# Kernel tuning notes

Measured on AMD Instinct MI355X. Metric: run time of the kernel, lower is better.

The kernel has to match this reference:

```python
import jax, jax.numpy as jnp
import numpy as np

EPS = 1e-5


def _gcn_conv(x, src, dst, n_nodes, W, b):
    # x: [N, Fin]; src/dst: [E+N] (self-loops already appended)
    h = x @ W                                   # [N, Fout]
    deg = jnp.zeros((n_nodes,), x.dtype).at[dst].add(1.0)
    dinv = jax.lax.rsqrt(deg)                   # deg >= 1 due to self-loops
    norm = dinv[src] * dinv[dst]                # [E+N]
    msg = h[src] * norm[:, None]                # [E+N, Fout]  (gather)
    out = jax.ops.segment_sum(msg, dst, num_segments=n_nodes)  # scatter-add
    return out + b


def _bn_relu(x, gamma, beta):
    # BatchNorm over nodes (training-style batch statistics), then ReLU.
    mu = jnp.mean(x, axis=0)
    var = jnp.mean((x - mu) ** 2, axis=0)       # biased variance (torch BN)
    xn = (x - mu) * jax.lax.rsqrt(var + EPS)
    return jax.nn.relu(xn * gamma + beta)


def setup_inputs() -> dict:
    key = jax.random.key(0)
    ks = jax.random.split(key, 12)
    N, E, Fin, H, O, G = 100000, 1600000, 128, 128, 64, 128
    x = jax.random.normal(ks[0], (N, Fin), dtype=jnp.float32)
    edge_index = jax.random.randint(ks[1], (2, E), 0, N, dtype=jnp.int64)
    batch = jnp.sort(jax.random.randint(ks[2], (N,), 0, G, dtype=jnp.int64))
    s = 1.0 / np.sqrt(Fin)
    W0 = jax.random.uniform(ks[3], (Fin, H), jnp.float32, -s, s)
    b0 = jnp.zeros((H,), jnp.float32)
    g0 = jnp.ones((H,), jnp.float32)
    be0 = jnp.zeros((H,), jnp.float32)
    s2 = 1.0 / np.sqrt(H)
    W1 = jax.random.uniform(ks[4], (H, H), jnp.float32, -s2, s2)
    b1 = jnp.zeros((H,), jnp.float32)
    g1 = jnp.ones((H,), jnp.float32)
    be1 = jnp.zeros((H,), jnp.float32)
    Wout = jax.random.uniform(ks[5], (H, O), jnp.float32, -s2, s2)
    bout = jax.random.uniform(ks[6], (O,), jnp.float32, -s2, s2)
    return {"x": x, "edge_index": edge_index, "batch": batch, "num_graphs": 128,
            "W0": W0, "b0": b0, "g0": g0, "be0": be0,
            "W1": W1, "b1": b1, "g1": g1, "be1": be1,
            "Wout": Wout, "bout": bout}


def reference(x, edge_index, batch, num_graphs,
              W0, b0, g0, be0, W1, b1, g1, be1, Wout, bout):
    N = x.shape[0]
    loops = jnp.arange(N, dtype=edge_index.dtype)
    src = jnp.concatenate([edge_index[0], loops])  # add self-loops
    dst = jnp.concatenate([edge_index[1], loops])
    h = _gcn_conv(x, src, dst, N, W0, b0)
    h = _bn_relu(h, g0, be0)                       # Dropout(p=0.1) = identity in eval
    h = _gcn_conv(h, src, dst, N, W1, b1)
    h = _bn_relu(h, g1, be1)
    # global mean pool over graphs
    sums = jax.ops.segment_sum(h, batch, num_segments=num_graphs)   # [G, H]
    cnt = jax.ops.segment_sum(jnp.ones((N,), h.dtype), batch, num_segments=num_graphs)
    pooled = sums / jnp.maximum(cnt, 1.0)[:, None]
    return pooled @ Wout + bout
```

## Files before the change

### kernel.cpp

```cpp
#include <hip/hip_runtime.h>
#include <hip/hip_bf16.h>

typedef _Float16 half8_t __attribute__((ext_vector_type(8)));
typedef _Float16 half2_t __attribute__((ext_vector_type(2)));
typedef float float4_t __attribute__((ext_vector_type(4)));
typedef float float2_t __attribute__((ext_vector_type(2)));

#define WROW 136


__global__ __launch_bounds__(256) void k_hist(const int* __restrict__ dst, int E, int SH,
                                              int NBK, int WG, int CH, int* __restrict__ M) {
    extern __shared__ int lh[];
    for (int i = threadIdx.x; i < NBK; i += 256) lh[i] = 0;
    __syncthreads();
    int wg = blockIdx.x;
    int e0 = wg * CH, e1 = min(E, e0 + CH);
    for (int e = e0 + threadIdx.x; e < e1; e += 256)
        atomicAdd(&lh[dst[e] >> SH], 1);
    __syncthreads();
    for (int i = threadIdx.x; i < NBK; i += 256) M[i * WG + wg] = lh[i];
}

__global__ __launch_bounds__(256) void k_colscan(int* __restrict__ M, int WG,
                                                 int* __restrict__ totals) {
    __shared__ int s[256];
    int b = blockIdx.x, t = threadIdx.x;
    int v = (t < WG) ? M[b * WG + t] : 0;
    s[t] = v;
    __syncthreads();
    for (int off = 1; off < 256; off <<= 1) {
        int u = (t >= off) ? s[t - off] : 0;
        __syncthreads();
        s[t] += u;
        __syncthreads();
    }
    if (t < WG) M[b * WG + t] = s[t] - v;
    if (t == 255) totals[b] = s[255];
}

__global__ __launch_bounds__(512) void k_bucketscan(const int* __restrict__ totals, int NBK,
                                                    int E, int* __restrict__ base) {
    __shared__ int s[512];
    int t = threadIdx.x;
    int v = (t < NBK) ? totals[t] : 0;
    s[t] = v;
    __syncthreads();
    for (int off = 1; off < 512; off <<= 1) {
        int u = (t >= off) ? s[t - off] : 0;
        __syncthreads();
        s[t] += u;
        __syncthreads();
    }
    if (t < NBK) base[t] = s[t] - v;
    if (t == 0) base[NBK] = E;
}

__global__ __launch_bounds__(256) void k_scatter(const int* __restrict__ src,
                                                 const int* __restrict__ dst, int E, int SH,
                                                 int NBK, int WG, int CH,
                                                 const int* __restrict__ M,
                                                 const int* __restrict__ base,
                                                 unsigned* __restrict__ ebuf) {
    extern __shared__ int cur[];
    int wg = blockIdx.x;
    for (int i = threadIdx.x; i < NBK; i += 256) cur[i] = base[i] + M[i * WG + wg];
    __syncthreads();
    int e0 = wg * CH, e1 = min(E, e0 + CH);
    for (int e = e0 + threadIdx.x; e < e1; e += 256) {
        int d = dst[e];
        int b = d >> SH;
        int pos = atomicAdd(&cur[b], 1);
        ebuf[pos] = (unsigned)src[e] | ((unsigned)(d - (b << SH)) << 23);
    }
}

__global__ __launch_bounds__(256) void k_cntfill(const unsigned* __restrict__ ebuf,
                                                 const int* __restrict__ base, int SH, int N,
                                                 int E, float* __restrict__ dinv,
                                                 int* __restrict__ rp, int* __restrict__ colx,
                                                 int* __restrict__ slots,
                                                 const float* __restrict__ W0,
                                                 const float* __restrict__ W1,
                                                 _Float16* __restrict__ Wt0,
                                                 _Float16* __restrict__ Wt1,
                                                 const int* __restrict__ batch, int G,
                                                 int* __restrict__ gptr,
                                                 float* __restrict__ psum,
                                                 float* __restrict__ sums,
                                                 unsigned char* __restrict__ A8) {
    __shared__ int h[512];
    __shared__ int cur[512];
    __shared__ int rs[512];
    __shared__ int lim[512];
    __shared__ int s[256];
    int b = blockIdx.x, t = threadIdx.x;

    if (b < 64) {
        int idx = b * 256 + t;
        int n = idx >> 7, k = idx & 127;
        Wt0[n * 128 + k] = (_Float16)W0[k * 128 + n];
        Wt1[n * 128 + k] = (_Float16)W1[k * 128 + n];
    } else if (b == 64) {
        if (t <= G) {
            int g = t;
            int lo = 0, hi = N;
            while (lo < hi) {
                int mid = (lo + hi) >> 1;
                if (batch[mid] < g) lo = mid + 1; else hi = mid;
            }
            gptr[g] = lo;
        }
    } else if (b < 97) {
        int i0 = (b - 65) * 512 + t;
        psum[i0] = 0.f;
        psum[i0 + 256] = 0.f;
    } else if (b == 97) {
        if (t < 256) { sums[t] = 0.f; sums[t + 256] = 0.f; }
        if (t < 32) ((unsigned*)A8)[(size_t)N * 32 + t] = 0u;
    }

    int n0 = b << SH;
    int nb = min(N - n0, 1 << SH);
    for (int i = t; i < nb; i += 256) h[i] = 0;
    __syncthreads();
    int e0 = base[b], e1 = base[b + 1];
    for (int e = e0 + t; e < e1; e += 256)
        atomicAdd(&h[ebuf[e] >> 23], 1);
    __syncthreads();
    int i0 = 2 * t, i1 = 2 * t + 1;
    int a0 = (i0 < nb) ? h[i0] : 0;
    int a1 = (i1 < nb) ? h[i1] : 0;
    int ps = a0 + a1;
    s[t] = ps;
    __syncthreads();
    for (int off = 1; off < 256; off <<= 1) {
        int u = (t >= off) ? s[t - off] : 0;
        __syncthreads();
        s[t] += u;
        __syncthreads();
    }
    int excl = s[t] - ps;
    if (i0 < nb) {
        int r0 = e0 + excl;
        cur[i0] = r0;
        rs[i0] = r0;
        lim[i0] = min(a0, 32);
        rp[n0 + i0] = r0;
        dinv[n0 + i0] = rsqrtf((float)(a0 + 1));
    }
    if (i1 < nb) {
        int r1 = e0 + excl + a0;
        cur[i1] = r1;
        rs[i1] = r1;
        lim[i1] = min(a1, 32);
        rp[n0 + i1] = r1;
        dinv[n0 + i1] = rsqrtf((float)(a1 + 1));
    }
    if (b == (int)gridDim.x - 1 && t == 0) rp[N] = E;
    __syncthreads();
    for (int e = e0 + t; e < e1; e += 256) {
        unsigned v = ebuf[e];
        int local = (int)(v >> 23);
        int srcn = (int)(v & 0x7FFFFFu);
        int pos = atomicAdd(&cur[local], 1);
        int off = pos - rs[local];
        if (slots && off < lim[local]) {
            int idx = ((off & 3) << 3) + (off >> 2);
            slots[(size_t)(n0 + local) * 32 + idx] = srcn;
        } else {
            colx[pos] = srcn;
        }
    }
}


__global__ __launch_bounds__(256) void k_gemmA(const float* __restrict__ X,
                                               const _Float16* __restrict__ Wt,
                                               const float* __restrict__ dinv,
                                               unsigned char* __restrict__ out, int N) {
    __shared__ _Float16 w[128 * WROW];
    int t = threadIdx.x;
    #pragma unroll
    for (int i = 0; i < 8; i++) {
        int idx = t + i * 256;
        int n = idx >> 4, k = (idx & 15) * 8;
        *(half8_t*)&w[n * WROW + k] = *(const half8_t*)(Wt + n * 128 + k);
    }
    __syncthreads();

    int wv = t >> 6, lane = t & 63;
    int m = lane & 15, quad = lane >> 4;
    int rowbase = blockIdx.x * 64 + wv * 16;
    int arow = rowbase + m;
    int arowc = (arow < N) ? arow : (N - 1);
    const float* xr = X + (size_t)arowc * 128;

    float4_t xa[4], xb[4];
    #pragma unroll
    for (int kc = 0; kc < 4; kc++) {
        xa[kc] = *(const float4_t*)(xr + kc * 32 + quad * 8);
        xb[kc] = *(const float4_t*)(xr + kc * 32 + quad * 8 + 4);
    }
    half8_t a[4];
    #pragma unroll
    for (int kc = 0; kc < 4; kc++) {
        #pragma unroll
        for (int j = 0; j < 4; j++) a[kc][j] = (_Float16)xa[kc][j];
        #pragma unroll
        for (int j = 0; j < 4; j++) a[kc][4 + j] = (_Float16)xb[kc][j];
    }

    float4_t acc[8];
    #pragma unroll
    for (int i = 0; i < 8; i++) acc[i] = (float4_t){0.f, 0.f, 0.f, 0.f};

    #pragma unroll
    for (int nt = 0; nt < 8; nt++) {
        const _Float16* wr = &w[(nt * 16 + m) * WROW + quad * 8];
        #pragma unroll
        for (int kc = 0; kc < 4; kc++) {
            half8_t b = *(const half8_t*)(wr + kc * 32);
            acc[nt] = __builtin_amdgcn_mfma_f32_16x16x32_f16(a[kc], b, acc[nt], 0, 0, 0);
        }
    }

    #pragma unroll
    for (int r = 0; r < 4; r++) {
        int row = rowbase + quad * 4 + r;
        if (row < N) {
            float dv = dinv[row];
            unsigned char* o = out + (size_t)row * 128 + m;
            #pragma unroll
            for (int nt = 0; nt < 8; nt++) {
                float v = acc[nt][r] * dv;
                int pk = __builtin_amdgcn_cvt_pk_fp8_f32(v, v, 0, false);
                o[nt * 16] = (unsigned char)(pk & 0xFF);
            }
        }
    }
}

__global__ __launch_bounds__(256) void k_gemmB(const _Float16* __restrict__ X,
                                               const _Float16* __restrict__ Wt,
                                               const float* __restrict__ sums,
                                               const float* __restrict__ g,
                                               const float* __restrict__ be,
                                               const float* __restrict__ dinv,
                                               unsigned char* __restrict__ out, int N) {
    __shared__ _Float16 w[128 * WROW];
    __shared__ alignas(16) float ss[128];
    __shared__ alignas(16) float hh[128];
    int t = threadIdx.x;
    if (t < 128) {
        float invN = 1.0f / (float)N;
        float mu = sums[t] * invN;
        float var = fmaxf(sums[128 + t] * invN - mu * mu, 0.f);
        float sc = g[t] * rsqrtf(var + 1e-5f);
        ss[t] = sc;
        hh[t] = fmaf(-mu, sc, be[t]);
    }
    #pragma unroll
    for (int i = 0; i < 8; i++) {
        int idx = t + i * 256;
        int n = idx >> 4, k = (idx & 15) * 8;
        *(half8_t*)&w[n * WROW + k] = *(const half8_t*)(Wt + n * 128 + k);
    }
    __syncthreads();

    int wv = t >> 6, lane = t & 63;
    int m = lane & 15, quad = lane >> 4;
    int rowbase = blockIdx.x * 64 + wv * 16;
    int arow = rowbase + m;
    int arowc = (arow < N) ? arow : (N - 1);
    const _Float16* xr = X + (size_t)arowc * 128;

    half8_t x8[4];
    #pragma unroll
    for (int kc = 0; kc < 4; kc++)
        x8[kc] = *(const half8_t*)(xr + kc * 32 + quad * 8);

    half8_t a[4];
    #pragma unroll
    for (int kc = 0; kc < 4; kc++) {
        int k0 = kc * 32 + quad * 8;
        float4_t sa = *(const float4_t*)(ss + k0);
        float4_t sb = *(const float4_t*)(ss + k0 + 4);
        float4_t ha = *(const float4_t*)(hh + k0);
        float4_t hb = *(const float4_t*)(hh + k0 + 4);
        #pragma unroll
        for (int j = 0; j < 4; j++)
            a[kc][j] = (_Float16)fmaxf(fmaf((float)x8[kc][j], sa[j], ha[j]), 0.f);
        #pragma unroll
        for (int j = 0; j < 4; j++)
            a[kc][4 + j] = (_Float16)fmaxf(fmaf((float)x8[kc][4 + j], sb[j], hb[j]), 0.f);
    }

    float4_t acc[8];
    #pragma unroll
    for (int i = 0; i < 8; i++) acc[i] = (float4_t){0.f, 0.f, 0.f, 0.f};

    #pragma unroll
    for (int nt = 0; nt < 8; nt++) {
        const _Float16* wr = &w[(nt * 16 + m) * WROW + quad * 8];
        #pragma unroll
        for (int kc = 0; kc < 4; kc++) {
            half8_t b = *(const half8_t*)(wr + kc * 32);
            acc[nt] = __builtin_amdgcn_mfma_f32_16x16x32_f16(a[kc], b, acc[nt], 0, 0, 0);
        }
    }

    #pragma unroll
    for (int r = 0; r < 4; r++) {
        int row = rowbase + quad * 4 + r;
        if (row < N) {
            float dv = dinv[row];
            unsigned char* o = out + (size_t)row * 128 + m;
            #pragma unroll
            for (int nt = 0; nt < 8; nt++) {
                float v = acc[nt][r] * dv;
                int pk = __builtin_amdgcn_cvt_pk_fp8_f32(v, v, 0, false);
                o[nt * 16] = (unsigned char)(pk & 0xFF);
            }
        }
    }
}


__device__ __forceinline__ void acc8(uint2 v, float2_t* a2) {
    a2[0] += __builtin_amdgcn_cvt_pk_f32_fp8((int)v.x, false);
    a2[1] += __builtin_amdgcn_cvt_pk_f32_fp8((int)v.x, true);
    a2[2] += __builtin_amdgcn_cvt_pk_f32_fp8((int)v.y, false);
    a2[3] += __builtin_amdgcn_cvt_pk_f32_fp8((int)v.y, true);
}

__device__ __forceinline__ void f8x4(unsigned w, float* o) {
    o[0] = __builtin_amdgcn_cvt_f32_fp8((int)w, 0);
    o[1] = __builtin_amdgcn_cvt_f32_fp8((int)w, 1);
    o[2] = __builtin_amdgcn_cvt_f32_fp8((int)w, 2);
    o[3] = __builtin_amdgcn_cvt_f32_fp8((int)w, 3);
}

__global__ __launch_bounds__(256) void k_aggS8(const unsigned char* __restrict__ hs,
                                               const int* __restrict__ slots,
                                               const int* __restrict__ rp,
                                               const int* __restrict__ colx,
                                               const float* __restrict__ bias,
                                               _Float16* __restrict__ out, int N) {
    int wave = (blockIdx.x * 256 + threadIdx.x) >> 6;
    int lane = threadIdx.x & 63;
    if (wave >= N) return;
    int i = wave;
    int q = lane >> 4;
    int c8 = lane & 15;

    const int4* sl4 = (const int4*)(slots + (size_t)i * 32 + 8 * q);
    int4 sa = sl4[0];
    int k0 = rp[i], k1 = rp[i + 1];
    uint2 sw = *(const uint2*)(hs + (size_t)i * 128 + c8 * 8);
    int deg = k1 - k0;

    float2_t a2[4] = {{0.f, 0.f}, {0.f, 0.f}, {0.f, 0.f}, {0.f, 0.f}};

    {
        int jraw[4] = {sa.x, sa.y, sa.z, sa.w};
        int j[4];
        #pragma unroll
        for (int s = 0; s < 4; s++)
            j[s] = (q + 4 * s < deg) ? jraw[s] : N;
        uint2 v[4];
        #pragma unroll
        for (int s = 0; s < 4; s++)
            v[s] = *(const uint2*)(hs + (size_t)j[s] * 128 + c8 * 8);
        #pragma unroll
        for (int s = 0; s < 4; s++) acc8(v[s], a2);
    }
    if (deg > 16) {
        int4 sb = sl4[1];
        int jraw[4] = {sb.x, sb.y, sb.z, sb.w};
        int j[4];
        #pragma unroll
        for (int s = 0; s < 4; s++)
            j[s] = (16 + q + 4 * s < deg) ? jraw[s] : N;
        uint2 v[4];
        #pragma unroll
        for (int s = 0; s < 4; s++)
            v[s] = *(const uint2*)(hs + (size_t)j[s] * 128 + c8 * 8);
        #pragma unroll
        for (int s = 0; s < 4; s++) acc8(v[s], a2);
        if (deg > 32) {
            for (int k = k0 + 32 + q; k < k1; k += 4) {
                uint2 vv = *(const uint2*)(hs + (size_t)colx[k] * 128 + c8 * 8);
                acc8(vv, a2);
            }
        }
    }

    float a[8] = {a2[0].x, a2[0].y, a2[1].x, a2[1].y,
                  a2[2].x, a2[2].y, a2[3].x, a2[3].y};
    #pragma unroll
    for (int t = 0; t < 8; t++) {
        float x = a[t];
        x += __shfl_xor(x, 16);
        x += __shfl_xor(x, 32);
        a[t] = x;
    }

    if (q == 0) {
        float d = rsqrtf((float)(deg + 1));
        float4 bA = ((const float4*)bias)[2 * c8];
        float4 bB = ((const float4*)bias)[2 * c8 + 1];
        float bb[8] = {bA.x, bA.y, bA.z, bA.w, bB.x, bB.y, bB.z, bB.w};
        float sf[8];
        f8x4(sw.x, sf);
        f8x4(sw.y, sf + 4);
        half8_t o;
        #pragma unroll
        for (int t = 0; t < 8; t++)
            o[t] = (_Float16)fmaf(a[t] + sf[t], d, bb[t]);
        ((half8_t*)out)[(size_t)i * 16 + c8] = o;
    }
}

__global__ __launch_bounds__(256) void k_aggC8(const unsigned char* __restrict__ hs,
                                               const int* __restrict__ rp,
                                               const int* __restrict__ colx,
                                               const float* __restrict__ bias,
                                               _Float16* __restrict__ out, int N) {
    int wave = (blockIdx.x * 256 + threadIdx.x) >> 6;
    int lane = threadIdx.x & 63;
    if (wave >= N) return;
    int i = wave;
    int q = lane >> 4;
    int c8 = lane & 15;

    uint2 sw = *(const uint2*)(hs + (size_t)i * 128 + c8 * 8);
    int k0 = rp[i], k1 = rp[i + 1];

    float2_t a2[4] = {{0.f, 0.f}, {0.f, 0.f}, {0.f, 0.f}, {0.f, 0.f}};
    for (int k = k0 + q; k < k1; k += 4) {
        uint2 vv = *(const uint2*)(hs + (size_t)colx[k] * 128 + c8 * 8);
        acc8(vv, a2);
    }

    float a[8] = {a2[0].x, a2[0].y, a2[1].x, a2[1].y,
                  a2[2].x, a2[2].y, a2[3].x, a2[3].y};
    #pragma unroll
    for (int t = 0; t < 8; t++) {
        float x = a[t];
        x += __shfl_xor(x, 16);
        x += __shfl_xor(x, 32);
        a[t] = x;
    }

    if (q == 0) {
        float d = rsqrtf((float)(k1 - k0 + 1));
        float4 bA = ((const float4*)bias)[2 * c8];
        float4 bB = ((const float4*)bias)[2 * c8 + 1];
        float bb[8] = {bA.x, bA.y, bA.z, bA.w, bB.x, bB.y, bB.z, bB.w};
        float sf[8];
        f8x4(sw.x, sf);
        f8x4(sw.y, sf + 4);
        half8_t o;
        #pragma unroll
        for (int t = 0; t < 8; t++)
            o[t] = (_Float16)fmaf(a[t] + sf[t], d, bb[t]);
        ((half8_t*)out)[(size_t)i * 16 + c8] = o;
    }
}


__global__ __launch_bounds__(256) void k_stats(const _Float16* __restrict__ x, int N,
                                               float* __restrict__ sums) {
    int lane = threadIdx.x & 63;
    int wv = threadIdx.x >> 6;
    int gw = blockIdx.x * 4 + wv;
    int stride = gridDim.x * 4;
    const half2_t* b = (const half2_t*)x;
    float2 s = make_float2(0.f, 0.f), q = make_float2(0.f, 0.f);
    for (int i = gw; i < N; i += stride) {
        half2_t v = b[(size_t)i * 64 + lane];
        float vx = (float)v.x, vy = (float)v.y;
        s.x += vx; s.y += vy;
        q.x += vx * vx; q.y += vy * vy;
    }
    __shared__ float ls[4][128];
    __shared__ float lq[4][128];
    ls[wv][2 * lane] = s.x; ls[wv][2 * lane + 1] = s.y;
    lq[wv][2 * lane] = q.x; lq[wv][2 * lane + 1] = q.y;
    __syncthreads();
    int t = threadIdx.x;
    if (t < 128) {
        float ts = ls[0][t] + ls[1][t] + ls[2][t] + ls[3][t];
        float tq = lq[0][t] + lq[1][t] + lq[2][t] + lq[3][t];
        atomicAdd(&sums[t], ts);
        atomicAdd(&sums[128 + t], tq);
    }
}


__global__ __launch_bounds__(256) void k_pool2(const _Float16* __restrict__ x,
                                               const int* __restrict__ batch,
                                               const float* __restrict__ sums,
                                               const float* __restrict__ g2,
                                               const float* __restrict__ be2,
                                               float* __restrict__ psum, int N) {
    __shared__ alignas(8) float ss[128];
    __shared__ alignas(8) float hh[128];
    int t = threadIdx.x;
    if (t < 128) {
        float invN = 1.0f / (float)N;
        float mu = sums[t] * invN;
        float var = fmaxf(sums[128 + t] * invN - mu * mu, 0.f);
        float sc = g2[t] * rsqrtf(var + 1e-5f);
        ss[t] = sc;
        hh[t] = fmaf(-mu, sc, be2[t]);
    }
    __syncthreads();

    int nw = gridDim.x * 4;
    int w = blockIdx.x * 4 + (threadIdx.x >> 6);
    int lane = threadIdx.x & 63;
    int per = (N + nw - 1) / nw;
    int i0 = w * per, i1 = min(N, i0 + per);
    if (i0 >= i1) return;
    const half2_t* b = (const half2_t*)x;
    float2 s2 = ((const float2*)ss)[lane];
    float2 h2 = ((const float2*)hh)[lane];
    float2 acc = make_float2(0.f, 0.f);
    int g = batch[i0];
    for (int i = i0; i < i1; i++) {
        int gi = batch[i];
        if (gi != g) {
            atomicAdd(&psum[g * 128 + 2 * lane], acc.x);
            atomicAdd(&psum[g * 128 + 2 * lane + 1], acc.y);
            acc = make_float2(0.f, 0.f);
            g = gi;
        }
        half2_t v = b[(size_t)i * 64 + lane];
        acc.x += fmaxf(fmaf((float)v.x, s2.x, h2.x), 0.f);
        acc.y += fmaxf(fmaf((float)v.y, s2.y, h2.y), 0.f);
    }
    atomicAdd(&psum[g * 128 + 2 * lane], acc.x);
    atomicAdd(&psum[g * 128 + 2 * lane + 1], acc.y);
}


__global__ __launch_bounds__(64) void k_final(const float* __restrict__ psum,
                                              const int* __restrict__ gptr,
                                              const float* __restrict__ Wout,
                                              const float* __restrict__ bout,
                                              float* __restrict__ out, int O) {
    int g = blockIdx.x, o = threadIdx.x;
    int cnt = gptr[g + 1] - gptr[g];
    float inv = 1.0f / fmaxf((float)cnt, 1.f);
    float acc = 0.f;
    for (int c = 0; c < 128; c++) acc = fmaf(psum[g * 128 + c], Wout[c * O + o], acc);
    out[g * O + o] = fmaf(acc, inv, bout[o]);
}


extern "C" void kernel_launch(void* const* d_in, const int* in_sizes, int n_in,
                              void* d_out, int out_size, void* d_ws, size_t ws_size,
                              hipStream_t stream) {
    const float* x    = (const float*)d_in[0];
    const int*   edge = (const int*)d_in[1];
    const int*   batch= (const int*)d_in[2];
    const float* W0   = (const float*)d_in[4];
    const float* b0   = (const float*)d_in[5];
    const float* g0   = (const float*)d_in[6];
    const float* be0  = (const float*)d_in[7];
    const float* W1   = (const float*)d_in[8];
    const float* b1   = (const float*)d_in[9];
    const float* g1   = (const float*)d_in[10];
    const float* be1  = (const float*)d_in[11];
    const float* Wout = (const float*)d_in[12];
    const float* bout = (const float*)d_in[13];
    float* out = (float*)d_out;

    const int Hh  = in_sizes[5];
    const int Fin = in_sizes[4] / Hh;
    const int N   = in_sizes[0] / Fin;
    const int E   = in_sizes[1] / 2;
    const int O   = in_sizes[13];
    const int G   = out_size / O;
    (void)Hh; (void)n_in;

    int SH = 8;
    while (((N + (1 << SH) - 1) >> SH) > 512) SH++;
    const int NBK = (N + (1 << SH) - 1) >> SH;
    const int CH  = ((E + 255) / 256 > 8192) ? (E + 255) / 256 : 8192;
    const int WG  = (E + CH - 1) / CH;

    char* p = (char*)d_ws;
    auto alloc = [&](size_t bytes) -> void* {
        void* r = (void*)p;
        p += (bytes + 255) & ~(size_t)255;
        return r;
    };
    unsigned char* A8 = (unsigned char*)alloc((size_t)(N + 1) * 128);
    _Float16* B   = (_Float16*)alloc((size_t)N * 128 * 2);
    float* dinv   = (float*)alloc((size_t)N * 4);
    int*   rp     = (int*)alloc((size_t)(N + 1) * 4);
    int*   colx   = (int*)alloc((size_t)E * 4);
    unsigned* ebuf= (unsigned*)alloc((size_t)E * 4);
    int*   M      = (int*)alloc((size_t)NBK * WG * 4);
    int*   totals = (int*)alloc((size_t)NBK * 4);
    int*   base   = (int*)alloc((size_t)(NBK + 1) * 4);
    float* sums   = (float*)alloc(512 * 4);
    int*   gptr   = (int*)alloc((size_t)(G + 1) * 4);
    float* psum   = (float*)alloc((size_t)G * 128 * 4);
    _Float16* Wt0 = (_Float16*)alloc(128 * 128 * 2);
    _Float16* Wt1 = (_Float16*)alloc(128 * 128 * 2);
    int*   slots  = (int*)alloc((size_t)N * 32 * 4);
    bool useSlots = ((size_t)(p - (char*)d_ws) <= ws_size);
    if (!useSlots) slots = nullptr;

    const int* src = edge;
    const int* dst = edge + E;

    k_hist<<<WG, 256, NBK * 4, stream>>>(dst, E, SH, NBK, WG, CH, M);
    k_colscan<<<NBK, 256, 0, stream>>>(M, WG, totals);
    k_bucketscan<<<1, 512, 0, stream>>>(totals, NBK, E, base);
    k_scatter<<<WG, 256, NBK * 4, stream>>>(src, dst, E, SH, NBK, WG, CH, M, base, ebuf);
    k_cntfill<<<NBK, 256, 0, stream>>>(ebuf, base, SH, N, E, dinv, rp, colx, slots,
                                       W0, W1, Wt0, Wt1, batch, G, gptr, psum, sums, A8);

    k_gemmA<<<(N + 63) / 64, 256, 0, stream>>>(x, Wt0, dinv, A8, N);
    if (useSlots)
        k_aggS8<<<(N + 3) / 4, 256, 0, stream>>>(A8, slots, rp, colx, b0, B, N);
    else
        k_aggC8<<<(N + 3) / 4, 256, 0, stream>>>(A8, rp, colx, b0, B, N);
    k_stats<<<512, 256, 0, stream>>>(B, N, sums);

    k_gemmB<<<(N + 63) / 64, 256, 0, stream>>>(B, Wt1, sums, g0, be0, dinv, A8, N);
    if (useSlots)
        k_aggS8<<<(N + 3) / 4, 256, 0, stream>>>(A8, slots, rp, colx, b1, B, N);
    else
        k_aggC8<<<(N + 3) / 4, 256, 0, stream>>>(A8, rp, colx, b1, B, N);
    k_stats<<<512, 256, 0, stream>>>(B, N, sums + 256);

    k_pool2<<<512, 256, 0, stream>>>(B, batch, sums + 256, g1, be1, psum, N);
    k_final<<<G, 64, 0, stream>>>(psum, gptr, Wout, bout, out, O);
}
```

Measured before the change: 355.0 us.

## Use finer CSR-build buckets and vectorize the BatchNorm stats reduction

```diff
diff --git a/kernel.cpp b/kernel.cpp
--- a/kernel.cpp
+++ b/kernel.cpp
@@ -39,14 +39,14 @@
     if (t == 255) totals[b] = s[255];
 }
 
-__global__ __launch_bounds__(512) void k_bucketscan(const int* __restrict__ totals, int NBK,
-                                                    int E, int* __restrict__ base) {
-    __shared__ int s[512];
+__global__ __launch_bounds__(1024) void k_bucketscan(const int* __restrict__ totals, int NBK,
+                                                     int E, int* __restrict__ base) {
+    __shared__ int s[1024];
     int t = threadIdx.x;
     int v = (t < NBK) ? totals[t] : 0;
     s[t] = v;
     __syncthreads();
-    for (int off = 1; off < 512; off <<= 1) {
+    for (int off = 1; off < 1024; off <<= 1) {
         int u = (t >= off) ? s[t - off] : 0;
         __syncthreads();
         s[t] += u;
@@ -89,10 +89,10 @@
                                                  float* __restrict__ psum,
                                                  float* __restrict__ sums,
                                                  unsigned char* __restrict__ A8) {
-    __shared__ int h[512];
-    __shared__ int cur[512];
-    __shared__ int rs[512];
-    __shared__ int lim[512];
+    __shared__ int h[128];
+    __shared__ int cur[128];
+    __shared__ int rs[128];
+    __shared__ int lim[128];
     __shared__ int s[256];
     int b = blockIdx.x, t = threadIdx.x;
 
@@ -122,7 +122,7 @@
 
     int n0 = b << SH;
     int nb = min(N - n0, 1 << SH);
-    for (int i = t; i < nb; i += 256) h[i] = 0;
+    if (t < 128 && t < nb) h[t] = 0;
     __syncthreads();
     int e0 = base[b], e1 = base[b + 1];
     for (int e = e0 + t; e < e1; e += 256)
@@ -472,24 +472,37 @@
 
 __global__ __launch_bounds__(256) void k_stats(const _Float16* __restrict__ x, int N,
                                                float* __restrict__ sums) {
-    int lane = threadIdx.x & 63;
-    int wv = threadIdx.x >> 6;
+    int t = threadIdx.x;
+    int lane = t & 63, wv = t >> 6;
+    int sub = lane >> 4, c8 = lane & 15;
     int gw = blockIdx.x * 4 + wv;
-    int stride = gridDim.x * 4;
-    const half2_t* b = (const half2_t*)x;
-    float2 s = make_float2(0.f, 0.f), q = make_float2(0.f, 0.f);
-    for (int i = gw; i < N; i += stride) {
-        half2_t v = b[(size_t)i * 64 + lane];
-        float vx = (float)v.x, vy = (float)v.y;
-        s.x += vx; s.y += vy;
-        q.x += vx * vx; q.y += vy * vy;
+    int rstride = gridDim.x * 4 * 4;
+    float s[8] = {0.f, 0.f, 0.f, 0.f, 0.f, 0.f, 0.f, 0.f};
+    float q[8] = {0.f, 0.f, 0.f, 0.f, 0.f, 0.f, 0.f, 0.f};
+    for (int row = gw * 4 + sub; row < N; row += rstride) {
+        half8_t v = *(const half8_t*)(x + (size_t)row * 128 + c8 * 8);
+        #pragma unroll
+        for (int j = 0; j < 8; j++) {
+            float f = (float)v[j];
+            s[j] += f;
+            q[j] += f * f;
+        }
+    }
+    #pragma unroll
+    for (int j = 0; j < 8; j++) {
+        s[j] += __shfl_xor(s[j], 16); s[j] += __shfl_xor(s[j], 32);
+        q[j] += __shfl_xor(q[j], 16); q[j] += __shfl_xor(q[j], 32);
     }
     __shared__ float ls[4][128];
     __shared__ float lq[4][128];
-    ls[wv][2 * lane] = s.x; ls[wv][2 * lane + 1] = s.y;
-    lq[wv][2 * lane] = q.x; lq[wv][2 * lane + 1] = q.y;
-    __syncthreads();
-    int t = threadIdx.x;
+    if (sub == 0) {
+        #pragma unroll
+        for (int j = 0; j < 8; j++) {
+            ls[wv][c8 * 8 + j] = s[j];
+            lq[wv][c8 * 8 + j] = q[j];
+        }
+    }
+    __syncthreads();
     if (t < 128) {
         float ts = ls[0][t] + ls[1][t] + ls[2][t] + ls[3][t];
         float tq = lq[0][t] + lq[1][t] + lq[2][t] + lq[3][t];
@@ -586,8 +599,8 @@
     const int G   = out_size / O;
     (void)Hh; (void)n_in;
 
-    int SH = 8;
-    while (((N + (1 << SH) - 1) >> SH) > 512) SH++;
+    int SH = 7;
+    while (((N + (1 << SH) - 1) >> SH) > 1024) SH++;
     const int NBK = (N + (1 << SH) - 1) >> SH;
     const int CH  = ((E + 255) / 256 > 8192) ? (E + 255) / 256 : 8192;
     const int WG  = (E + CH - 1) / CH;
@@ -621,7 +634,7 @@
 
     k_hist<<<WG, 256, NBK * 4, stream>>>(dst, E, SH, NBK, WG, CH, M);
     k_colscan<<<NBK, 256, 0, stream>>>(M, WG, totals);
-    k_bucketscan<<<1, 512, 0, stream>>>(totals, NBK, E, base);
+    k_bucketscan<<<1, 1024, 0, stream>>>(totals, NBK, E, base);
     k_scatter<<<WG, 256, NBK * 4, stream>>>(src, dst, E, SH, NBK, WG, CH, M, base, ebuf);
     k_cntfill<<<NBK, 256, 0, stream>>>(ebuf, base, SH, N, E, dinv, rp, colx, slots,
                                        W0, W1, Wt0, Wt1, batch, G, gptr, psum, sums, A8);
```

Result: faster. 339.4 us (-4.4%).
